# Performance work log

Hardware: AMD Instinct MI355X
Metric: run time of the kernel (lower is better)

Reference implementation:

```python
import jax, jax.numpy as jnp
import numpy as np

N = 8192  # NBNEUR (scaled from original 1001 for production scale)


def setup_inputs() -> dict:
    key = jax.random.key(0)
    k1, k2, k3, k4 = jax.random.split(key, 4)
    return {
        "input": jax.random.normal(k1, (1, N), dtype=jnp.float32),
        "yin": jax.random.normal(k2, (1, N), dtype=jnp.float32),
        "hebb": jnp.zeros((N, N), dtype=jnp.float32),
        "w": 0.01 * jax.random.normal(k3, (N, N), dtype=jnp.float32),
        "alpha": 0.01 * jax.random.normal(k4, (N, N), dtype=jnp.float32),
        "eta": 0.01 * jnp.ones((1,), dtype=jnp.float32),
    }


def reference(input, yin, hebb, w, alpha, eta):
    # yout = tanh(yin @ (w + alpha * hebb) + input)   -> [1, N]
    yout = jnp.tanh(yin @ (w + alpha * hebb) + input)
    # Hebbian update: decay + outer product of pre (yin) and post (yout)
    # torch.bmm(yin.unsqueeze(2), yout.unsqueeze(1))[0] == outer(yin[0], yout[0])
    hebb_new = (1.0 - eta) * hebb + eta * (yin[0][:, None] * yout[0][None, :])
    return (yout, hebb_new)
```

## Files before the change

### kernel.cpp

```cpp
#include <hip/hip_runtime.h>

#define NN 8192

__global__ __launch_bounds__(256) void init_z(const float* __restrict__ input,
                                              float* __restrict__ z) {
    int j = blockIdx.x * 256 + threadIdx.x;
    z[j] = input[j];
}

__global__ __launch_bounds__(256) void matvec_partial(
    const float* __restrict__ yin,
    const float* __restrict__ w,
    const float* __restrict__ alpha,
    const float* __restrict__ hebb,
    float* __restrict__ z)
{
    const int j0 = blockIdx.x * 1024 + threadIdx.x * 4;
    const int i0 = blockIdx.y * 128;

    float4 s = make_float4(0.f, 0.f, 0.f, 0.f);
    for (int r = 0; r < 128; ++r) {
        const int i = i0 + r;
        const float y = yin[i];
        const size_t base = (size_t)i * NN + (size_t)j0;
        const float4 wv = *(const float4*)(w + base);
        const float4 av = *(const float4*)(alpha + base);
        const float4 hv = *(const float4*)(hebb + base);
        s.x = fmaf(y, fmaf(av.x, hv.x, wv.x), s.x);
        s.y = fmaf(y, fmaf(av.y, hv.y, wv.y), s.y);
        s.z = fmaf(y, fmaf(av.z, hv.z, wv.z), s.z);
        s.w = fmaf(y, fmaf(av.w, hv.w, wv.w), s.w);
    }
    atomicAdd(&z[j0 + 0], s.x);
    atomicAdd(&z[j0 + 1], s.y);
    atomicAdd(&z[j0 + 2], s.z);
    atomicAdd(&z[j0 + 3], s.w);
}

__global__ __launch_bounds__(256) void tanh_k(const float* __restrict__ z,
                                              float* __restrict__ yout) {
    int j = blockIdx.x * 256 + threadIdx.x;
    yout[j] = tanhf(z[j]);
}

__global__ __launch_bounds__(256) void hebb_update(
    const float* __restrict__ hebb,
    const float* __restrict__ yin,
    const float* __restrict__ yout,
    const float* __restrict__ eta_p,
    float* __restrict__ hebb_out)
{
    const float eta = eta_p[0];
    const float om = 1.0f - eta;
    const size_t f0 = (size_t)blockIdx.x * 1024 + threadIdx.x;
#pragma unroll
    for (int k = 0; k < 4; ++k) {
        const size_t f = f0 + (size_t)k * 256;
        const size_t i = f >> 11;
        const size_t j = (f & 2047) * 4;
        const float ye = eta * yin[i];
        const float4 h  = *(const float4*)(hebb + i * NN + j);
        const float4 yo = *(const float4*)(yout + j);
        float4 o;
        o.x = fmaf(om, h.x, ye * yo.x);
        o.y = fmaf(om, h.y, ye * yo.y);
        o.z = fmaf(om, h.z, ye * yo.z);
        o.w = fmaf(om, h.w, ye * yo.w);
        *(float4*)(hebb_out + i * NN + j) = o;
    }
}

extern "C" void kernel_launch(void* const* d_in, const int* in_sizes, int n_in,
                              void* d_out, int out_size, void* d_ws, size_t ws_size,
                              hipStream_t stream) {
    const float* input = (const float*)d_in[0];
    const float* yin   = (const float*)d_in[1];
    const float* hebb  = (const float*)d_in[2];
    const float* w     = (const float*)d_in[3];
    const float* alpha = (const float*)d_in[4];
    const float* eta   = (const float*)d_in[5];

    float* yout_out = (float*)d_out;
    float* hebb_out = yout_out + NN;
    float* z = (float*)d_ws;

    init_z<<<NN / 256, 256, 0, stream>>>(input, z);
    matvec_partial<<<dim3(8, 64), 256, 0, stream>>>(yin, w, alpha, hebb, z);
    tanh_k<<<NN / 256, 256, 0, stream>>>(z, yout_out);
    hebb_update<<<(NN * (size_t)NN) / 4096, 256, 0, stream>>>(hebb, yin, yout_out, eta, hebb_out);
}
```

Before: 802.9 us.

## Retile matvec: more row blocks and four column chunks per thread

The matvec kernel goes from an 8x64 grid, where each thread sums 128 rows for 4 columns, to a 2x1024 grid, where each thread sums 8 rows for 16 columns in four float4 chunks. Twelve independent float4 loads are issued per row iteration. The aim is to raise the number of blocks and the memory-level parallelism on a bandwidth-bound read of three 256MB matrices. The cost is 16x more atomicAdds into z and more registers per thread.

```diff
diff --git a/kernel.cpp b/kernel.cpp
--- a/kernel.cpp
+++ b/kernel.cpp
@@ -15,26 +15,42 @@
     const float* __restrict__ hebb,
     float* __restrict__ z)
 {
-    const int j0 = blockIdx.x * 1024 + threadIdx.x * 4;
-    const int i0 = blockIdx.y * 128;
+    const int j0 = blockIdx.x * 4096 + threadIdx.x * 4;
+    const int i0 = blockIdx.y * 8;
 
-    float4 s = make_float4(0.f, 0.f, 0.f, 0.f);
-    for (int r = 0; r < 128; ++r) {
+    float4 s[4];
+#pragma unroll
+    for (int c = 0; c < 4; ++c) s[c] = make_float4(0.f, 0.f, 0.f, 0.f);
+
+    for (int r = 0; r < 8; ++r) {
         const int i = i0 + r;
         const float y = yin[i];
         const size_t base = (size_t)i * NN + (size_t)j0;
-        const float4 wv = *(const float4*)(w + base);
-        const float4 av = *(const float4*)(alpha + base);
-        const float4 hv = *(const float4*)(hebb + base);
-        s.x = fmaf(y, fmaf(av.x, hv.x, wv.x), s.x);
-        s.y = fmaf(y, fmaf(av.y, hv.y, wv.y), s.y);
-        s.z = fmaf(y, fmaf(av.z, hv.z, wv.z), s.z);
-        s.w = fmaf(y, fmaf(av.w, hv.w, wv.w), s.w);
+
+        float4 wv[4], av[4], hv[4];
+#pragma unroll
+        for (int c = 0; c < 4; ++c) wv[c] = *(const float4*)(w + base + c * 1024);
+#pragma unroll
+        for (int c = 0; c < 4; ++c) av[c] = *(const float4*)(alpha + base + c * 1024);
+#pragma unroll
+        for (int c = 0; c < 4; ++c) hv[c] = *(const float4*)(hebb + base + c * 1024);
+
+#pragma unroll
+        for (int c = 0; c < 4; ++c) {
+            s[c].x = fmaf(y, fmaf(av[c].x, hv[c].x, wv[c].x), s[c].x);
+            s[c].y = fmaf(y, fmaf(av[c].y, hv[c].y, wv[c].y), s[c].y);
+            s[c].z = fmaf(y, fmaf(av[c].z, hv[c].z, wv[c].z), s[c].z);
+            s[c].w = fmaf(y, fmaf(av[c].w, hv[c].w, wv[c].w), s[c].w);
+        }
     }
-    atomicAdd(&z[j0 + 0], s.x);
-    atomicAdd(&z[j0 + 1], s.y);
-    atomicAdd(&z[j0 + 2], s.z);
-    atomicAdd(&z[j0 + 3], s.w);
+
+#pragma unroll
+    for (int c = 0; c < 4; ++c) {
+        atomicAdd(&z[j0 + c * 1024 + 0], s[c].x);
+        atomicAdd(&z[j0 + c * 1024 + 1], s[c].y);
+        atomicAdd(&z[j0 + c * 1024 + 2], s[c].z);
+        atomicAdd(&z[j0 + c * 1024 + 3], s[c].w);
+    }
 }
 
 __global__ __launch_bounds__(256) void tanh_k(const float* __restrict__ z,
@@ -85,7 +101,7 @@
     float* z = (float*)d_ws;
 
     init_z<<<NN / 256, 256, 0, stream>>>(input, z);
-    matvec_partial<<<dim3(8, 64), 256, 0, stream>>>(yin, w, alpha, hebb, z);
+    matvec_partial<<<dim3(2, 1024), 256, 0, stream>>>(yin, w, alpha, hebb, z);
     tanh_k<<<NN / 256, 256, 0, stream>>>(z, yout_out);
     hebb_update<<<(NN * (size_t)NN) / 4096, 256, 0, stream>>>(hebb, yin, yout_out, eta, hebb_out);
 }
```

Result: slower. 826.1 us (+2.9%).
